# Kernel optimization log

Measured on AMD Instinct MI355X. Metric: run time of the kernel, lower is better.

Reference implementation:

```python
import jax, jax.numpy as jnp
import numpy as np

B, T, D_IN, D_OUT = 4, 2048, 1024, 1024

def setup_inputs() -> dict:
    key = jax.random.key(0)
    k1, k2, k3, k4 = jax.random.split(key, 4)
    return {
        "vector": jax.random.normal(k1, (B, T, D_IN), dtype=jnp.float32),
        "W_queries": jax.random.normal(k2, (D_IN, D_OUT), dtype=jnp.float32),
        "W_keys": jax.random.normal(k3, (D_IN, D_OUT), dtype=jnp.float32),
        "W_values": jax.random.normal(k4, (D_IN, D_OUT), dtype=jnp.float32),
    }

def reference(vector, W_queries, W_keys, W_values):
    # vector: [B,T,d_in]; projections -> [B,T,d_out]
    q = vector @ W_queries
    k = vector @ W_keys
    v = vector @ W_values
    d_out = k.shape[-1]
    scores = jnp.einsum('btd,bsd->bts', q, k)  # [B,T,T]
    t = scores.shape[1]
    causal = jnp.tril(jnp.ones((t, t), dtype=bool))  # True = keep (mask is triu diag=1)
    scores = jnp.where(causal, scores, -jnp.inf)
    weights = jax.nn.softmax(scores / jnp.sqrt(jnp.float32(d_out)), axis=-1)
    # dropout p=0.0 -> identity
    return jnp.einsum('bts,bsd->btd', weights, v)
```

## Files before the change

### kernel.cpp

```cpp
#include <hip/hip_runtime.h>

#define TT   2048
#define DD   1024
#define BK   32

typedef float  f32x4  __attribute__((ext_vector_type(4)));
typedef __bf16 bf16x8 __attribute__((ext_vector_type(8)));

static __device__ __forceinline__ unsigned short f2bf(float f){
  unsigned int u = __float_as_uint(f);
  return (unsigned short)((u + 0x7fffu + ((u >> 16) & 1u)) >> 16);
}
static __device__ __forceinline__ float bf2f(unsigned short h){
  return __uint_as_float(((unsigned int)h) << 16);
}
static __device__ __forceinline__ bf16x8 ld8(const unsigned short* p){
  return *(const bf16x8*)p;
}
static __device__ __forceinline__ f32x4 mfma16(bf16x8 a, bf16x8 b, f32x4 c){
  return __builtin_amdgcn_mfma_f32_16x16x32_bf16(a, b, c, 0, 0, 0);
}

static __device__ __forceinline__ void async16(
    const unsigned short* g, unsigned short* l)
{
  __builtin_amdgcn_global_load_lds(
      (const __attribute__((address_space(1))) unsigned int*)g,
      (__attribute__((address_space(3))) unsigned int*)l, 16, 0, 0);
}

static __device__ __forceinline__ void stage_async(
    const unsigned short* __restrict__ src, int row_stride,
    unsigned short* __restrict__ dst, int t)
{
#pragma unroll
  for (int j = 0; j < 2; j++){
    int e = (t + j * 256) * 8;
    int row = e >> 5, col = e & 31;
    async16(src + (size_t)row * row_stride + col, dst + e);
  }
}

static __device__ __forceinline__ void stage_async64(
    const unsigned short* __restrict__ src, int row_stride,
    unsigned short* __restrict__ dst, int t)
{
#pragma unroll
  for (int j = 0; j < 4; j++){
    int e = (t + j * 256) * 8;
    int row = e >> 6, cs = (e >> 3) & 7;
    int srcc = cs ^ (row & 7);
    async16(src + (size_t)row * row_stride + srcc * 8, dst + e);
  }
}
static __device__ __forceinline__ bf16x8 ld8sw(
    const unsigned short* tile, int row, int c)
{
  return ld8(&tile[row * 64 + ((c ^ (row & 7)) << 3)]);
}

__global__ __launch_bounds__(256) void split_all_kernel(
    const float* __restrict__ X,  const float* __restrict__ Wq,
    const float* __restrict__ Wk, const float* __restrict__ Wv,
    unsigned short* __restrict__ Xhi,  unsigned short* __restrict__ Xlo,
    unsigned short* __restrict__ Wqhi, unsigned short* __restrict__ Wqlo,
    unsigned short* __restrict__ Wkhi, unsigned short* __restrict__ Wklo,
    unsigned short* __restrict__ WvThi)
{
  __shared__ float tile[32][33];
  int bx = blockIdx.x;
  if (bx < 10240){
    const float* src; unsigned short *hi, *lo; size_t base;
    if (bx < 8192)      { src = X;  hi = Xhi;  lo = Xlo;  base = (size_t)bx * 1024; }
    else if (bx < 9216) { src = Wq; hi = Wqhi; lo = Wqlo; base = (size_t)(bx - 8192) * 1024; }
    else                { src = Wk; hi = Wkhi; lo = Wklo; base = (size_t)(bx - 9216) * 1024; }
    size_t i = base + (size_t)threadIdx.x * 4;
    const float4 x = *(const float4*)(src + i);
    ushort4 h, l;
    h.x = f2bf(x.x); l.x = f2bf(x.x - bf2f(h.x));
    h.y = f2bf(x.y); l.y = f2bf(x.y - bf2f(h.y));
    h.z = f2bf(x.z); l.z = f2bf(x.z - bf2f(h.z));
    h.w = f2bf(x.w); l.w = f2bf(x.w - bf2f(h.w));
    *(ushort4*)(hi + i) = h;
    *(ushort4*)(lo + i) = l;
  } else {
    int tid = bx - 10240;
    int k0 = (tid & 31) * 32, n0 = (tid >> 5) * 32;
    int tx = threadIdx.x & 31, ty = threadIdx.x >> 5;
#pragma unroll
    for (int r = 0; r < 4; r++){
      int row = ty + r * 8;
      tile[row][tx] = Wv[(size_t)(k0 + row) * DD + n0 + tx];
    }
    __syncthreads();
#pragma unroll
    for (int r = 0; r < 4; r++){
      int nrow = ty + r * 8;
      float v = tile[tx][nrow];
      WvThi[(size_t)(n0 + nrow) * DD + k0 + tx] = f2bf(v);
    }
  }
}

__global__ __launch_bounds__(256) void mt_kernel(
    const unsigned short* __restrict__ Wkhi, const unsigned short* __restrict__ Wklo,
    const unsigned short* __restrict__ Wqhi, const unsigned short* __restrict__ Wqlo,
    unsigned short* __restrict__ MThi, unsigned short* __restrict__ MTlo)
{
  __shared__ unsigned short Ahi[128 * BK], Alo[128 * BK];
  __shared__ unsigned short Bhi[128 * BK], Blo[128 * BK];
  int e0 = blockIdx.y * 128, d0 = blockIdx.x * 128;
  const unsigned short* Ah_g = Wkhi + (size_t)e0 * DD;
  const unsigned short* Al_g = Wklo + (size_t)e0 * DD;
  const unsigned short* Bh_g = Wqhi + (size_t)d0 * DD;
  const unsigned short* Bl_g = Wqlo + (size_t)d0 * DD;
  int t = threadIdx.x;
  int lane = t & 63, w = t >> 6;
  int mw = (w >> 1) << 6, nw = (w & 1) << 6;
  int frow = lane & 15, fk = (lane >> 4) << 3;

  f32x4 acc[4][4];
#pragma unroll
  for (int a = 0; a < 4; a++)
#pragma unroll
    for (int c = 0; c < 4; c++){ f32x4 zz = {0.f,0.f,0.f,0.f}; acc[a][c] = zz; }

  for (int kk = 0; kk < DD / BK; kk++){
    int k0 = kk * BK;
    stage_async(Ah_g + k0, DD, Ahi, t);
    stage_async(Al_g + k0, DD, Alo, t);
    stage_async(Bh_g + k0, DD, Bhi, t);
    stage_async(Bl_g + k0, DD, Blo, t);
    __syncthreads();

    bf16x8 ah[4], al[4], bh[4], bl[4];
#pragma unroll
    for (int tm = 0; tm < 4; tm++){
      int off = (mw + tm * 16 + frow) * BK + fk;
      ah[tm] = ld8(&Ahi[off]); al[tm] = ld8(&Alo[off]);
    }
#pragma unroll
    for (int tn = 0; tn < 4; tn++){
      int off = (nw + tn * 16 + frow) * BK + fk;
      bh[tn] = ld8(&Bhi[off]); bl[tn] = ld8(&Blo[off]);
    }
#pragma unroll
    for (int tm = 0; tm < 4; tm++)
#pragma unroll
      for (int tn = 0; tn < 4; tn++){
        acc[tm][tn] = mfma16(ah[tm], bh[tn], acc[tm][tn]);
        acc[tm][tn] = mfma16(ah[tm], bl[tn], acc[tm][tn]);
        acc[tm][tn] = mfma16(al[tm], bh[tn], acc[tm][tn]);
      }
    __syncthreads();
  }

#pragma unroll
  for (int tm = 0; tm < 4; tm++)
#pragma unroll
    for (int tn = 0; tn < 4; tn++)
#pragma unroll
      for (int r = 0; r < 4; r++){
        float v = acc[tm][tn][r];
        int ge = e0 + mw + tm * 16 + ((lane >> 4) << 2) + r;
        int gd = d0 + nw + tn * 16 + frow;
        size_t idx = (size_t)ge * DD + gd;
        unsigned short h = f2bf(v);
        MThi[idx] = h; MTlo[idx] = f2bf(v - bf2f(h));
      }
}

__global__ __launch_bounds__(256, 2) void y_kernel(
    const unsigned short* __restrict__ Xhi, const unsigned short* __restrict__ Xlo,
    const unsigned short* __restrict__ MThi, const unsigned short* __restrict__ MTlo,
    const unsigned short* __restrict__ WvThi,
    unsigned short* __restrict__ Yhi, unsigned short* __restrict__ Ylo,
    unsigned short* __restrict__ VT)
{
  __shared__ unsigned short pool[40960];
  unsigned short* Ahs = pool;
  unsigned short* Als = pool + 8192;
  unsigned short* Bmh = pool + 16384;
  unsigned short* Bml = pool + 24576;
  unsigned short* Bvh = pool + 32768;
  int m0 = blockIdx.x * 128, n0 = blockIdx.y * 128;
  const unsigned short* Ah_g  = Xhi   + (size_t)m0 * DD;
  const unsigned short* Al_g  = Xlo   + (size_t)m0 * DD;
  const unsigned short* Bmh_g = MThi  + (size_t)n0 * DD;
  const unsigned short* Bml_g = MTlo  + (size_t)n0 * DD;
  const unsigned short* Bvh_g = WvThi + (size_t)n0 * DD;
  int t = threadIdx.x;
  int lane = t & 63, w = t >> 6;
  int mw = (w >> 1) << 6, nw = (w & 1) << 6;
  int frow = lane & 15, fk = (lane >> 4) << 3;
  int fc = fk >> 3;

  f32x4 accY[4][4], accV[4][4];
#pragma unroll
  for (int a = 0; a < 4; a++)
#pragma unroll
    for (int c = 0; c < 4; c++){
      f32x4 zz = {0.f,0.f,0.f,0.f}; accY[a][c] = zz; accV[a][c] = zz;
    }

  for (int kk = 0; kk < DD / 64; kk++){
    int k0 = kk * 64;
    stage_async64(Ah_g  + k0, DD, Ahs, t);
    stage_async64(Al_g  + k0, DD, Als, t);
    stage_async64(Bmh_g + k0, DD, Bmh, t);
    stage_async64(Bml_g + k0, DD, Bml, t);
    stage_async64(Bvh_g + k0, DD, Bvh, t);
    __syncthreads();

#pragma unroll
    for (int h = 0; h < 2; h++){
      int cb = h * 4 + fc;
      bf16x8 ah[4], al[4];
#pragma unroll
      for (int tm = 0; tm < 4; tm++){
        int row = mw + tm * 16 + frow;
        ah[tm] = ld8sw(Ahs, row, cb); al[tm] = ld8sw(Als, row, cb);
      }
#pragma unroll
      for (int tn = 0; tn < 4; tn++){
        int rowb = nw + tn * 16 + frow;
        bf16x8 bmh = ld8sw(Bmh, rowb, cb);
        bf16x8 bml = ld8sw(Bml, rowb, cb);
        bf16x8 bvh = ld8sw(Bvh, rowb, cb);
#pragma unroll
        for (int tm = 0; tm < 4; tm++){
          accY[tm][tn] = mfma16(ah[tm], bmh, accY[tm][tn]);
          accY[tm][tn] = mfma16(ah[tm], bml, accY[tm][tn]);
          accY[tm][tn] = mfma16(al[tm], bmh, accY[tm][tn]);
          accV[tm][tn] = mfma16(ah[tm], bvh, accV[tm][tn]);
        }
      }
    }
    __syncthreads();
  }

#pragma unroll
  for (int tm = 0; tm < 4; tm++)
#pragma unroll
    for (int tn = 0; tn < 4; tn++)
#pragma unroll
      for (int r = 0; r < 4; r++){
        int grow = m0 + mw + tm * 16 + ((lane >> 4) << 2) + r;
        int gcol = n0 + nw + tn * 16 + frow;
        size_t idx = (size_t)grow * DD + gcol;
        float vy = accY[tm][tn][r];
        unsigned short hy = f2bf(vy);
        Yhi[idx] = hy; Ylo[idx] = f2bf(vy - bf2f(hy));
      }

#pragma unroll
  for (int tm = 0; tm < 4; tm++)
#pragma unroll
    for (int tn = 0; tn < 4; tn++){
      int row = mw + tm * 16 + ((lane >> 4) << 2);
      int col = nw + tn * 16 + frow;
      ushort4 v4;
      v4.x = f2bf(accV[tm][tn][0]);
      v4.y = f2bf(accV[tm][tn][1]);
      v4.z = f2bf(accV[tm][tn][2]);
      v4.w = f2bf(accV[tm][tn][3]);
      *(ushort4*)&pool[col * 132 + row] = v4;
    }
  __syncthreads();
  {
    int colx = t >> 1;
    int r0 = (t & 1) << 6;
    int b = m0 >> 11;
    size_t vbase = (((size_t)(b * DD + n0 + colx)) << 11) | ((size_t)(m0 & 2047) + r0);
    const unsigned short* srcl = &pool[colx * 132 + r0];
#pragma unroll
    for (int r = 0; r < 64; r += 4)
      *(ushort4*)&VT[vbase + r] = *(const ushort4*)&srcl[r];
  }
}

__global__ __launch_bounds__(256) void s_kernel(
    const unsigned short* __restrict__ Yhi, const unsigned short* __restrict__ Ylo,
    const unsigned short* __restrict__ Xhi, const unsigned short* __restrict__ Xlo,
    float* __restrict__ S, float* __restrict__ Spart)
{
  __shared__ unsigned short pool[32768];
  unsigned short* Ahi = pool;
  unsigned short* Alo = pool + 8192;
  unsigned short* Bhi = pool + 16384;
  unsigned short* Blo = pool + 24576;
  int bx = blockIdx.x;
  int u, q, kbeg, kend;
  if (bx < 512){ u = bx; q = 0; kbeg = 0; kend = 16; }
  else {
    int e = bx - 512;
    q = e & 3;
    u = 512 + (e >> 2);
    kbeg = q * 4; kend = kbeg + 4;
  }
  int b = u & 3;
  int tid = u >> 2;
  int bi = (int)((sqrtf(8.f * (float)tid + 1.f) - 1.f) * 0.5f);
  while ((bi + 1) * (bi + 2) / 2 <= tid) bi++;
  while (bi * (bi + 1) / 2 > tid) bi--;
  int bj = tid - bi * (bi + 1) / 2;
  int i0 = bi * 128, j0 = bj * 128;
  const unsigned short* Ah_g = Yhi + (size_t)(b * TT + i0) * DD;
  const unsigned short* Al_g = Ylo + (size_t)(b * TT + i0) * DD;
  const unsigned short* Bh_g = Xhi + (size_t)(b * TT + j0) * DD;
  const unsigned short* Bl_g = Xlo + (size_t)(b * TT + j0) * DD;
  int t = threadIdx.x;
  int lane = t & 63, w = t >> 6;
  int mw = (w >> 1) << 6, nw = (w & 1) << 6;
  int frow = lane & 15, fk = (lane >> 4) << 3;
  int fc = fk >> 3;

  f32x4 acc[4][4];
#pragma unroll
  for (int a = 0; a < 4; a++)
#pragma unroll
    for (int c = 0; c < 4; c++){ f32x4 zz = {0.f,0.f,0.f,0.f}; acc[a][c] = zz; }

  for (int kk = kbeg; kk < kend; kk++){
    int k0 = kk * 64;
    stage_async64(Ah_g + k0, DD, Ahi, t);
    stage_async64(Al_g + k0, DD, Alo, t);
    stage_async64(Bh_g + k0, DD, Bhi, t);
    stage_async64(Bl_g + k0, DD, Blo, t);
    __syncthreads();

#pragma unroll
    for (int h = 0; h < 2; h++){
      int cb = h * 4 + fc;
      bf16x8 ah[4], al[4], bh[4], bl[4];
#pragma unroll
      for (int tm = 0; tm < 4; tm++){
        int row = mw + tm * 16 + frow;
        ah[tm] = ld8sw(Ahi, row, cb); al[tm] = ld8sw(Alo, row, cb);
      }
#pragma unroll
      for (int tn = 0; tn < 4; tn++){
        int rowb = nw + tn * 16 + frow;
        bh[tn] = ld8sw(Bhi, rowb, cb); bl[tn] = ld8sw(Blo, rowb, cb);
      }
#pragma unroll
      for (int tm = 0; tm < 4; tm++)
#pragma unroll
        for (int tn = 0; tn < 4; tn++){
          acc[tm][tn] = mfma16(ah[tm], bh[tn], acc[tm][tn]);
          acc[tm][tn] = mfma16(ah[tm], bl[tn], acc[tm][tn]);
          acc[tm][tn] = mfma16(al[tm], bh[tn], acc[tm][tn]);
        }
    }
    __syncthreads();
  }

  if (q == 0){
#pragma unroll
    for (int tm = 0; tm < 4; tm++)
#pragma unroll
      for (int tn = 0; tn < 4; tn++)
#pragma unroll
        for (int r = 0; r < 4; r++){
          int gi = i0 + mw + tm * 16 + ((lane >> 4) << 2) + r;
          int gj = j0 + nw + tn * 16 + frow;
          S[((size_t)(b * TT + gi) * TT) + gj] = acc[tm][tn][r] * 0.03125f;
        }
  } else {
    float* dst = Spart + ((size_t)(q - 1) * 32 + (u - 512)) * 16384;
#pragma unroll
    for (int tm = 0; tm < 4; tm++)
#pragma unroll
      for (int tn = 0; tn < 4; tn++)
#pragma unroll
        for (int r = 0; r < 4; r++){
          int row = mw + tm * 16 + ((lane >> 4) << 2) + r;
          int col = nw + tn * 16 + frow;
          dst[row * 128 + col] = acc[tm][tn][r] * 0.03125f;
        }
  }
}

__global__ __launch_bounds__(256) void softmax_kernel(
    const float* __restrict__ S, const float* __restrict__ Spart,
    unsigned short* __restrict__ P)
{
  int i = blockIdx.x, b = blockIdx.y;
  const float* s = S + (size_t)(b * TT + i) * TT;
  unsigned short* p = P + (size_t)(b * TT + i) * TT;
  int n = i + 1;
  int npad = ((i >> 7) + 1) << 7;
  int t = threadIdx.x;
  bool qrow = (i >= 1920);
  __shared__ float red[256];

  float v[8];
  float mx = -1e30f;
#pragma unroll
  for (int pas = 0; pas < 2; pas++){
    int idx = t * 4 + pas * 1024;
    float4 x = {-1e30f, -1e30f, -1e30f, -1e30f};
    if (idx < npad){
      x = *(const float4*)(s + idx);
      if (qrow && pas == 1){
        int jt = (idx - 1024) >> 7;
        int qt = 4 * jt + b;
        size_t base = (size_t)qt * 16384 + (size_t)(i - 1920) * 128 + ((idx - 1024) & 127);
        const float4 p1 = *(const float4*)(Spart + base);
        const float4 p2 = *(const float4*)(Spart + 32 * 16384 + base);
        const float4 p3 = *(const float4*)(Spart + 2 * 32 * 16384 + base);
        x.x += p1.x + p2.x + p3.x;
        x.y += p1.y + p2.y + p3.y;
        x.z += p1.z + p2.z + p3.z;
        x.w += p1.w + p2.w + p3.w;
      }
    }
    v[pas*4+0] = (idx + 0 < n) ? x.x : -1e30f;
    v[pas*4+1] = (idx + 1 < n) ? x.y : -1e30f;
    v[pas*4+2] = (idx + 2 < n) ? x.z : -1e30f;
    v[pas*4+3] = (idx + 3 < n) ? x.w : -1e30f;
#pragma unroll
    for (int e = 0; e < 4; e++) mx = fmaxf(mx, v[pas*4+e]);
  }
  red[t] = mx; __syncthreads();
  for (int k = 128; k > 0; k >>= 1){ if (t < k) red[t] = fmaxf(red[t], red[t + k]); __syncthreads(); }
  mx = red[0]; __syncthreads();

  float sum = 0.f;
#pragma unroll
  for (int j = 0; j < 8; j++){
    v[j] = __expf(v[j] - mx);
    sum += v[j];
  }
  red[t] = sum; __syncthreads();
  for (int k = 128; k > 0; k >>= 1){ if (t < k) red[t] += red[t + k]; __syncthreads(); }
  float inv = 1.0f / red[0];

#pragma unroll
  for (int pas = 0; pas < 2; pas++){
    int idx = t * 4 + pas * 1024;
    if (idx < npad){
      ushort4 o;
      o.x = f2bf(v[pas*4+0] * inv);
      o.y = f2bf(v[pas*4+1] * inv);
      o.z = f2bf(v[pas*4+2] * inv);
      o.w = f2bf(v[pas*4+3] * inv);
      *(ushort4*)(p + idx) = o;
    }
  }
}

__global__ __launch_bounds__(256) void pv_kernel(
    const unsigned short* __restrict__ P, const unsigned short* __restrict__ VT,
    float* __restrict__ O)
{
  __shared__ unsigned short At0[128 * BK], At1[128 * BK];
  __shared__ unsigned short Bt0[128 * BK], Bt1[128 * BK];
  int b  = blockIdx.z;
  int by = (int)gridDim.y - 1 - blockIdx.y;
  int i0 = by * 128, n0 = blockIdx.x * 128;
  int ksteps = (by + 1) * 4;
  const unsigned short* A_g = P  + (size_t)(b * TT + i0) * TT;
  const unsigned short* B_g = VT + (size_t)(b * DD + n0) * TT;
  int t = threadIdx.x;
  int lane = t & 63, w = t >> 6;
  int mw = (w >> 1) << 6, nw = (w & 1) << 6;
  int frow = lane & 15, fk = (lane >> 4) << 3;

  f32x4 acc[4][4];
#pragma unroll
  for (int a = 0; a < 4; a++)
#pragma unroll
    for (int c = 0; c < 4; c++){ f32x4 zz = {0.f,0.f,0.f,0.f}; acc[a][c] = zz; }

  for (int kk = 0; kk < ksteps; kk += 2){
    int k0 = kk * BK;
    stage_async(A_g + k0, TT, At0, t);
    stage_async(A_g + k0 + BK, TT, At1, t);
    stage_async(B_g + k0, TT, Bt0, t);
    stage_async(B_g + k0 + BK, TT, Bt1, t);
    __syncthreads();

    bf16x8 af[4], bf[4];
#pragma unroll
    for (int tm = 0; tm < 4; tm++) af[tm] = ld8(&At0[(mw + tm * 16 + frow) * BK + fk]);
#pragma unroll
    for (int tn = 0; tn < 4; tn++) bf[tn] = ld8(&Bt0[(nw + tn * 16 + frow) * BK + fk]);
#pragma unroll
    for (int tm = 0; tm < 4; tm++)
#pragma unroll
      for (int tn = 0; tn < 4; tn++)
        acc[tm][tn] = mfma16(af[tm], bf[tn], acc[tm][tn]);
#pragma unroll
    for (int tm = 0; tm < 4; tm++) af[tm] = ld8(&At1[(mw + tm * 16 + frow) * BK + fk]);
#pragma unroll
    for (int tn = 0; tn < 4; tn++) bf[tn] = ld8(&Bt1[(nw + tn * 16 + frow) * BK + fk]);
#pragma unroll
    for (int tm = 0; tm < 4; tm++)
#pragma unroll
      for (int tn = 0; tn < 4; tn++)
        acc[tm][tn] = mfma16(af[tm], bf[tn], acc[tm][tn]);
    __syncthreads();
  }

#pragma unroll
  for (int tm = 0; tm < 4; tm++)
#pragma unroll
    for (int tn = 0; tn < 4; tn++)
#pragma unroll
      for (int r = 0; r < 4; r++){
        int gi = i0 + mw + tm * 16 + ((lane >> 4) << 2) + r;
        int gd = n0 + nw + tn * 16 + frow;
        O[(size_t)(b * TT + gi) * DD + gd] = acc[tm][tn][r];
      }
}

extern "C" void kernel_launch(void* const* d_in, const int* in_sizes, int n_in,
                              void* d_out, int out_size, void* d_ws, size_t ws_size,
                              hipStream_t stream) {
  const float* X  = (const float*)d_in[0];
  const float* Wq = (const float*)d_in[1];
  const float* Wk = (const float*)d_in[2];
  const float* Wv = (const float*)d_in[3];
  float* Out = (float*)d_out;

  const size_t M1 = 1048576u;
  unsigned short* base  = (unsigned short*)d_ws;
  unsigned short* Wqhi  = base;
  unsigned short* Wqlo  = base + 1 * M1;
  unsigned short* Wkhi  = base + 2 * M1;
  unsigned short* Wklo  = base + 3 * M1;
  unsigned short* WvThi = base + 4 * M1;
  unsigned short* MThi  = base + 5 * M1;
  unsigned short* MTlo  = base + 6 * M1;
  unsigned short* Xhi   = base + 7 * M1;
  unsigned short* Xlo   = base + 15 * M1;
  unsigned short* Yhi   = base + 23 * M1;
  unsigned short* Ylo   = base + 31 * M1;
  unsigned short* VT    = base + 39 * M1;
  float*          S     = (float*)(base + 47 * M1);
  float*          Spart = (float*)(base + 79 * M1);
  unsigned short* P     = Xhi;

  dim3 blk(256);
  split_all_kernel<<<dim3(11264), blk, 0, stream>>>(X, Wq, Wk, Wv,
      Xhi, Xlo, Wqhi, Wqlo, Wkhi, Wklo, WvThi);
  mt_kernel<<<dim3(8, 8), blk, 0, stream>>>(Wkhi, Wklo, Wqhi, Wqlo, MThi, MTlo);
  y_kernel<<<dim3(64, 8), blk, 0, stream>>>(Xhi, Xlo, MThi, MTlo, WvThi, Yhi, Ylo, VT);
  s_kernel<<<dim3(640), blk, 0, stream>>>(Yhi, Ylo, Xhi, Xlo, S, Spart);
  softmax_kernel<<<dim3(2048, 4, 1), blk, 0, stream>>>(S, Spart, P);
  pv_kernel<<<dim3(8, 16, 4), blk, 0, stream>>>(P, VT, Out);
}
```

Before: 304.1 us.

## Use 64-wide swizzled LDS K-tiles in mt and pv GEMM kernels

The 32-column unswizzled LDS staging in mt_kernel and pv_kernel is replaced with 64-column tiles loaded via stage_async64 and read with an XOR-swizzled ld8sw. This halves the number of barrier-separated iterations per K range and aims to remove LDS bank conflicts on the fragment reads. Both kernels now use a 64 KB shared pool, up from 32 KB, which can lower the number of resident blocks per CU.

```diff
diff --git a/kernel.cpp b/kernel.cpp
--- a/kernel.cpp
+++ b/kernel.cpp
@@ -27,18 +27,6 @@
   __builtin_amdgcn_global_load_lds(
       (const __attribute__((address_space(1))) unsigned int*)g,
       (__attribute__((address_space(3))) unsigned int*)l, 16, 0, 0);
-}
-
-static __device__ __forceinline__ void stage_async(
-    const unsigned short* __restrict__ src, int row_stride,
-    unsigned short* __restrict__ dst, int t)
-{
-#pragma unroll
-  for (int j = 0; j < 2; j++){
-    int e = (t + j * 256) * 8;
-    int row = e >> 5, col = e & 31;
-    async16(src + (size_t)row * row_stride + col, dst + e);
-  }
 }
 
 static __device__ __forceinline__ void stage_async64(
@@ -107,8 +95,11 @@
     const unsigned short* __restrict__ Wqhi, const unsigned short* __restrict__ Wqlo,
     unsigned short* __restrict__ MThi, unsigned short* __restrict__ MTlo)
 {
-  __shared__ unsigned short Ahi[128 * BK], Alo[128 * BK];
-  __shared__ unsigned short Bhi[128 * BK], Blo[128 * BK];
+  __shared__ unsigned short pool[32768];
+  unsigned short* Ahi = pool;
+  unsigned short* Alo = pool + 8192;
+  unsigned short* Bhi = pool + 16384;
+  unsigned short* Blo = pool + 24576;
   int e0 = blockIdx.y * 128, d0 = blockIdx.x * 128;
   const unsigned short* Ah_g = Wkhi + (size_t)e0 * DD;
   const unsigned short* Al_g = Wklo + (size_t)e0 * DD;
@@ -118,6 +109,7 @@
   int lane = t & 63, w = t >> 6;
   int mw = (w >> 1) << 6, nw = (w & 1) << 6;
   int frow = lane & 15, fk = (lane >> 4) << 3;
+  int fc = fk >> 3;
 
   f32x4 acc[4][4];
 #pragma unroll
@@ -125,33 +117,37 @@
 #pragma unroll
     for (int c = 0; c < 4; c++){ f32x4 zz = {0.f,0.f,0.f,0.f}; acc[a][c] = zz; }
 
-  for (int kk = 0; kk < DD / BK; kk++){
-    int k0 = kk * BK;
-    stage_async(Ah_g + k0, DD, Ahi, t);
-    stage_async(Al_g + k0, DD, Alo, t);
-    stage_async(Bh_g + k0, DD, Bhi, t);
-    stage_async(Bl_g + k0, DD, Blo, t);
-    __syncthreads();
-
-    bf16x8 ah[4], al[4], bh[4], bl[4];
-#pragma unroll
-    for (int tm = 0; tm < 4; tm++){
-      int off = (mw + tm * 16 + frow) * BK + fk;
-      ah[tm] = ld8(&Ahi[off]); al[tm] = ld8(&Alo[off]);
-    }
-#pragma unroll
-    for (int tn = 0; tn < 4; tn++){
-      int off = (nw + tn * 16 + frow) * BK + fk;
-      bh[tn] = ld8(&Bhi[off]); bl[tn] = ld8(&Blo[off]);
-    }
-#pragma unroll
-    for (int tm = 0; tm < 4; tm++)
+  for (int kk = 0; kk < DD / 64; kk++){
+    int k0 = kk * 64;
+    stage_async64(Ah_g + k0, DD, Ahi, t);
+    stage_async64(Al_g + k0, DD, Alo, t);
+    stage_async64(Bh_g + k0, DD, Bhi, t);
+    stage_async64(Bl_g + k0, DD, Blo, t);
+    __syncthreads();
+
+#pragma unroll
+    for (int h = 0; h < 2; h++){
+      int cb = h * 4 + fc;
+      bf16x8 ah[4], al[4], bh[4], bl[4];
+#pragma unroll
+      for (int tm = 0; tm < 4; tm++){
+        int row = mw + tm * 16 + frow;
+        ah[tm] = ld8sw(Ahi, row, cb); al[tm] = ld8sw(Alo, row, cb);
+      }
 #pragma unroll
       for (int tn = 0; tn < 4; tn++){
-        acc[tm][tn] = mfma16(ah[tm], bh[tn], acc[tm][tn]);
-        acc[tm][tn] = mfma16(ah[tm], bl[tn], acc[tm][tn]);
-        acc[tm][tn] = mfma16(al[tm], bh[tn], acc[tm][tn]);
-      }
+        int rowb = nw + tn * 16 + frow;
+        bh[tn] = ld8sw(Bhi, rowb, cb); bl[tn] = ld8sw(Blo, rowb, cb);
+      }
+#pragma unroll
+      for (int tm = 0; tm < 4; tm++)
+#pragma unroll
+        for (int tn = 0; tn < 4; tn++){
+          acc[tm][tn] = mfma16(ah[tm], bh[tn], acc[tm][tn]);
+          acc[tm][tn] = mfma16(ah[tm], bl[tn], acc[tm][tn]);
+          acc[tm][tn] = mfma16(al[tm], bh[tn], acc[tm][tn]);
+        }
+    }
     __syncthreads();
   }
 
@@ -454,18 +450,22 @@
     const unsigned short* __restrict__ P, const unsigned short* __restrict__ VT,
     float* __restrict__ O)
 {
-  __shared__ unsigned short At0[128 * BK], At1[128 * BK];
-  __shared__ unsigned short Bt0[128 * BK], Bt1[128 * BK];
+  __shared__ unsigned short pool[32768];
+  unsigned short* At0 = pool;
+  unsigned short* Bt0 = pool + 8192;
+  unsigned short* At1 = pool + 16384;
+  unsigned short* Bt1 = pool + 24576;
   int b  = blockIdx.z;
   int by = (int)gridDim.y - 1 - blockIdx.y;
   int i0 = by * 128, n0 = blockIdx.x * 128;
-  int ksteps = (by + 1) * 4;
+  int ksteps64 = (by + 1) * 2;
   const unsigned short* A_g = P  + (size_t)(b * TT + i0) * TT;
   const unsigned short* B_g = VT + (size_t)(b * DD + n0) * TT;
   int t = threadIdx.x;
   int lane = t & 63, w = t >> 6;
   int mw = (w >> 1) << 6, nw = (w & 1) << 6;
   int frow = lane & 15, fk = (lane >> 4) << 3;
+  int fc = fk >> 3;
 
   f32x4 acc[4][4];
 #pragma unroll
@@ -473,33 +473,33 @@
 #pragma unroll
     for (int c = 0; c < 4; c++){ f32x4 zz = {0.f,0.f,0.f,0.f}; acc[a][c] = zz; }
 
-  for (int kk = 0; kk < ksteps; kk += 2){
-    int k0 = kk * BK;
-    stage_async(A_g + k0, TT, At0, t);
-    stage_async(A_g + k0 + BK, TT, At1, t);
-    stage_async(B_g + k0, TT, Bt0, t);
-    stage_async(B_g + k0 + BK, TT, Bt1, t);
-    __syncthreads();
-
-    bf16x8 af[4], bf[4];
-#pragma unroll
-    for (int tm = 0; tm < 4; tm++) af[tm] = ld8(&At0[(mw + tm * 16 + frow) * BK + fk]);
-#pragma unroll
-    for (int tn = 0; tn < 4; tn++) bf[tn] = ld8(&Bt0[(nw + tn * 16 + frow) * BK + fk]);
-#pragma unroll
-    for (int tm = 0; tm < 4; tm++)
-#pragma unroll
-      for (int tn = 0; tn < 4; tn++)
-        acc[tm][tn] = mfma16(af[tm], bf[tn], acc[tm][tn]);
-#pragma unroll
-    for (int tm = 0; tm < 4; tm++) af[tm] = ld8(&At1[(mw + tm * 16 + frow) * BK + fk]);
-#pragma unroll
-    for (int tn = 0; tn < 4; tn++) bf[tn] = ld8(&Bt1[(nw + tn * 16 + frow) * BK + fk]);
-#pragma unroll
-    for (int tm = 0; tm < 4; tm++)
-#pragma unroll
-      for (int tn = 0; tn < 4; tn++)
-        acc[tm][tn] = mfma16(af[tm], bf[tn], acc[tm][tn]);
+  for (int kk = 0; kk < ksteps64; kk += 2){
+    int k0 = kk * 64;
+    stage_async64(A_g + k0, TT, At0, t);
+    stage_async64(B_g + k0, TT, Bt0, t);
+    stage_async64(A_g + k0 + 64, TT, At1, t);
+    stage_async64(B_g + k0 + 64, TT, Bt1, t);
+    __syncthreads();
+
+#pragma unroll
+    for (int sstep = 0; sstep < 2; sstep++){
+      const unsigned short* At = sstep ? At1 : At0;
+      const unsigned short* Bt = sstep ? Bt1 : Bt0;
+#pragma unroll
+      for (int h = 0; h < 2; h++){
+        int cb = h * 4 + fc;
+        bf16x8 af[4], bf[4];
+#pragma unroll
+        for (int tm = 0; tm < 4; tm++) af[tm] = ld8sw(At, mw + tm * 16 + frow, cb);
+#pragma unroll
+        for (int tn = 0; tn < 4; tn++) bf[tn] = ld8sw(Bt, nw + tn * 16 + frow, cb);
+#pragma unroll
+        for (int tm = 0; tm < 4; tm++)
+#pragma unroll
+          for (int tn = 0; tn < 4; tn++)
+            acc[tm][tn] = mfma16(af[tm], bf[tn], acc[tm][tn]);
+      }
+    }
     __syncthreads();
   }
 
```

Result: faster. 292.3 us (-3.9%).
